# Performance work log

Hardware: AMD Instinct MI355X
Metric: run time of the kernel (lower is better)

## Reference

```python
import jax, jax.numpy as jnp
from jax import lax
import numpy as np

NUM_ANCHORS = 3
NUM_CLASSES = 20
IMG_DIM = 416.0
ANCHORS = np.array([[10.0, 13.0], [16.0, 30.0], [33.0, 23.0]], dtype=np.float32)
BN_EPS = 1e-5


def setup_inputs() -> dict:
    key = jax.random.key(0)
    ks = jax.random.split(key, 8)
    B, Cin, G = 16, 256, 52
    Cmid = 2 * Cin
    Cout = NUM_ANCHORS * (NUM_CLASSES + 5)
    # weights scaled down so exp() in the box decode stays numerically tame
    return {
        "x": jax.random.normal(ks[0], (B, Cin, G, G), jnp.float32),
        "conv1_w": jax.random.normal(ks[1], (Cmid, Cin, 3, 3), jnp.float32) * 0.05,
        "bn_gamma": jnp.ones((Cmid,), jnp.float32),
        "bn_beta": jnp.zeros((Cmid,), jnp.float32),
        "bn_mean": jax.random.normal(ks[2], (Cmid,), jnp.float32) * 0.05,
        "bn_var": jax.random.uniform(ks[3], (Cmid,), jnp.float32, 0.5, 1.5),
        "conv2_w": jax.random.normal(ks[4], (Cout, Cmid, 1, 1), jnp.float32) * 0.05,
        "conv2_b": jnp.zeros((Cout,), jnp.float32),
    }


def _conv(x, w, padding):
    return lax.conv_general_dilated(
        x, w, window_strides=(1, 1), padding=padding,
        dimension_numbers=("NCHW", "OIHW", "NCHW"))


def reference(x, conv1_w, bn_gamma, bn_beta, bn_mean, bn_var, conv2_w, conv2_b):
    # BasicConv: conv3x3 (no bias) -> BatchNorm (inference stats) -> LeakyReLU(0.1)
    y = _conv(x, conv1_w, ((1, 1), (1, 1)))
    inv = bn_gamma / jnp.sqrt(bn_var + BN_EPS)
    y = y * inv[None, :, None, None] + (bn_beta - bn_mean * inv)[None, :, None, None]
    y = jnp.where(y > 0, y, 0.1 * y)
    # 1x1 head conv with bias
    y = _conv(y, conv2_w, ((0, 0), (0, 0))) + conv2_b[None, :, None, None]

    B, G = y.shape[0], y.shape[2]
    A, NC = NUM_ANCHORS, NUM_CLASSES
    # [B, A, 5+NC, G, G] -> [B, A, G, G, 5+NC]
    pred = y.reshape(B, A, NC + 5, G, G).transpose(0, 1, 3, 4, 2)

    obj_score = jax.nn.sigmoid(pred[..., 4])        # [B,A,G,G]
    pred_cls = jax.nn.sigmoid(pred[..., 5:])        # [B,A,G,G,NC]

    stride = IMG_DIM / G
    grid = jnp.arange(G, dtype=jnp.float32)
    grid_x = grid[None, None, None, :]              # [1,1,1,G]
    grid_y = grid[None, None, :, None]              # [1,1,G,1]
    scaled = jnp.asarray(ANCHORS) / stride          # [A,2]
    anchor_w = scaled[:, 0].reshape(1, A, 1, 1)
    anchor_h = scaled[:, 1].reshape(1, A, 1, 1)

    # original uses .data (detached) for box decode
    box_in = lax.stop_gradient(pred[..., :4])
    bx = jax.nn.sigmoid(box_in[..., 0]) + grid_x
    by = jax.nn.sigmoid(box_in[..., 1]) + grid_y
    bw = jnp.exp(box_in[..., 2]) * anchor_w
    bh = jnp.exp(box_in[..., 3]) * anchor_h
    pred_boxes = jnp.stack([bx, by, bw, bh], axis=-1) * stride  # [B,A,G,G,4]

    return jnp.concatenate(
        [pred_boxes.reshape(B, -1, 4),
         obj_score.reshape(B, -1, 1),
         pred_cls.reshape(B, -1, NC)], axis=-1)
```

## Files before the change

### kernel.cpp

```cpp
#include <hip/hip_runtime.h>

typedef _Float16 f16;
typedef _Float16 f16x8 __attribute__((ext_vector_type(8)));
typedef _Float16 f16x4 __attribute__((ext_vector_type(4)));
typedef float f32x4 __attribute__((ext_vector_type(4)));

#define GDIM 52
#define GG 2704
#define CIN 256
#define CMID 512
#define COUT 75
#define NIMG 16
#define SPT 192
#define NSPB 15
#define PH 60
#define PW 54

#define AT_OFF 0
#define AT_SZ 16384
#define SLAB_OFF 65536
#define SLAB_SZ 32768

#define VMCNT(n) asm volatile("s_waitcnt vmcnt(" #n ")" ::: "memory")

__device__ __forceinline__ float sigmoidf_(float x) {
    return 1.0f / (1.0f + __expf(-x));
}

__device__ __forceinline__ void gload16(const void* g, void* l) {
    __builtin_amdgcn_global_load_lds(
        (const __attribute__((address_space(1))) unsigned int*)g,
        (__attribute__((address_space(3))) unsigned int*)l, 16, 0, 0);
}

__global__ __launch_bounds__(256) void k_zero_border(f16* __restrict__ x16p) {
    int ic = blockIdx.x;
    int tid = threadIdx.x;
    f16x8 z;
#pragma unroll
    for (int k = 0; k < 8; ++k) z[k] = (f16)0;
    for (int j = tid; j < 536; j += 256) {
        int row, col;
        if (j < 432) { int r = j / 54; row = (r == 0) ? 0 : 52 + r; col = j % 54; }
        else { int k = j - 432; row = 1 + (k >> 1); col = (k & 1) * 53; }
        f16* p = x16p + (((size_t)ic * PH + row) * PW + col) * 32;
#pragma unroll
        for (int q = 0; q < 4; ++q) *(f16x8*)(p + q * 8) = z;
    }
}

__global__ __launch_bounds__(256) void k_prep_x(const float* __restrict__ x,
                                                f16* __restrict__ x16p) {
    __shared__ float ls[32][133];
    int hw0 = blockIdx.x * 128, ck = blockIdx.y, img = blockIdx.z;
    int tid = threadIdx.x;
    const float* xb = x + ((size_t)img * CIN + ck * 32) * GG;
#pragma unroll
    for (int i = 0; i < 16; ++i) {
        int idx = tid + i * 256;
        int r = idx >> 7, c = idx & 127;
        int hw = hw0 + c;
        ls[r][c] = (hw < GG) ? xb[(size_t)r * GG + hw] : 0.0f;
    }
    __syncthreads();
    int col = tid >> 1, half = tid & 1;
    int hw = hw0 + col;
    if (hw < GG) {
        int h = hw / GDIM, w = hw % GDIM;
        f16* dst = x16p + ((((size_t)img * 8 + ck) * PH + h + 1) * PW + (w + 1)) * 32 + half * 16;
        f16x8 o0, o1;
#pragma unroll
        for (int j = 0; j < 8; ++j) o0[j] = (f16)ls[half * 16 + j][col];
#pragma unroll
        for (int j = 0; j < 8; ++j) o1[j] = (f16)ls[half * 16 + 8 + j][col];
        *(f16x8*)dst = o0;
        *(f16x8*)(dst + 8) = o1;
    }
}

__global__ __launch_bounds__(256) void k_prep_w(
    const float* __restrict__ w1, const float* __restrict__ w2,
    const float* __restrict__ gamma, const float* __restrict__ beta,
    const float* __restrict__ mean, const float* __restrict__ var,
    f16* __restrict__ w16, f16* __restrict__ w2_16,
    float* __restrict__ bnscale, float* __restrict__ bnshift) {
    int i = blockIdx.x * 256 + threadIdx.x;
    int cl = i & 31;
    int co = (i >> 5) & 511;
    int ckt = i >> 14;
    int ck = ckt & 7, tap = ckt >> 3;
    int ci = ck * 32 + cl;
    w16[i] = (f16)w1[(size_t)co * 2304 + ci * 9 + tap];
    if (i < COUT * CMID) w2_16[i] = (f16)w2[i];
    if (i < CMID) {
        float s = gamma[i] * rsqrtf(var[i] + 1e-5f);
        bnscale[i] = s;
        bnshift[i] = beta[i] - mean[i] * s;
    }
}

__global__ __launch_bounds__(512, 2) void k_conv1(
    const f16* __restrict__ x16p, const f16* __restrict__ w16,
    const float* __restrict__ bnscale, const float* __restrict__ bnshift,
    f16* __restrict__ y16) {
    __shared__ __align__(16) char smem[131072];
    int img = blockIdx.x / NSPB, sb = blockIdx.x % NSPB;
    int n0 = sb * SPT;
    int h_lo = n0 / GDIM;
    int half = blockIdx.y;
    int co0 = half * 256;
    int tid = threadIdx.x;
    int lane = tid & 63, wave = tid >> 6;
    int wm = wave >> 1, wn = wave & 1;
    int l15 = lane & 15, kg = lane >> 4;

    int roff[6];
#pragma unroll
    for (int nf = 0; nf < 6; ++nf) {
        int n = n0 + wn * 96 + nf * 16 + l15;
        int nc = n < GG ? n : GG - 1;
        int hh = nc / GDIM, ww = nc % GDIM;
        roff[nf] = ((hh - h_lo + 1) * PW + (ww + 1)) * 8;
    }

    f32x4 acc[4][6];
#pragma unroll
    for (int a = 0; a < 4; ++a)
#pragma unroll
        for (int b = 0; b < 6; ++b) {
            acc[a][b][0] = 0.f; acc[a][b][1] = 0.f;
            acc[a][b][2] = 0.f; acc[a][b][3] = 0.f;
        }

    const f16* xbase = x16p + ((size_t)img * 8 * PH + h_lo) * (PW * 32);
    f16x8 fa[2][4], fb[2][6];

    {
        const f16* wA0 = w16 + (size_t)co0 * 32;
        f16* d0 = (f16*)(smem + AT_OFF);
#pragma unroll
        for (int p = 0; p < 2; ++p) {
            int u = p * 512 + tid, s = u >> 8, c = u & 255;
            gload16(wA0 + (size_t)c * 32 + s * 8, d0 + (size_t)u * 8);
        }
        f16* sd = (f16*)(smem + SLAB_OFF);
#pragma unroll
        for (int p = 0; p < 4; ++p) {
            int cix = p * 512 + tid;
            int pix = cix & 511; if (pix > 377) pix = 377;
            gload16(xbase + (size_t)pix * 32 + (cix >> 9) * 8, sd + (size_t)cix * 8);
        }
        const f16* wA1 = w16 + ((size_t)8 * 512 + co0) * 32;
        f16* d1 = (f16*)(smem + AT_OFF + AT_SZ);
#pragma unroll
        for (int p = 0; p < 2; ++p) {
            int u = p * 512 + tid, s = u >> 8, c = u & 255;
            gload16(wA1 + (size_t)c * 32 + s * 8, d1 + (size_t)u * 8);
        }
    }
    VMCNT(2);
    __builtin_amdgcn_s_barrier();
    __builtin_amdgcn_sched_barrier(0);
    {
        const f16* Ab = (const f16*)(smem + AT_OFF);
        const f16* Sb = (const f16*)(smem + SLAB_OFF);
        const int tappix = -PW - 1;
#pragma unroll
        for (int mf = 0; mf < 4; ++mf)
            fa[0][mf] = *(const f16x8*)(Ab + kg * 2048 + (wm * 64 + l15) * 8 + mf * 128);
#pragma unroll
        for (int nf = 0; nf < 6; ++nf)
            fb[0][nf] = *(const f16x8*)(Sb + kg * 4096 + roff[nf] + tappix * 8);
    }
    __builtin_amdgcn_sched_barrier(0);

    for (int q = 0; q < 2; ++q) {
#pragma unroll
        for (int u = 0; u < 36; ++u) {
            if (u == 1 || u == 10 || u == 19 || u == 28) {
                int ckS = q * 4 + u / 9 + 1;
                const f16* sg;
                f16* sd;
                if (ckS > 7) {
                    sg = xbase + (size_t)7 * (PH * PW * 32);
                    sd = (f16*)(smem + AT_OFF + ((u + 2) % 4) * AT_SZ);
                } else {
                    sg = xbase + (size_t)ckS * (PH * PW * 32);
                    sd = (f16*)(smem + SLAB_OFF + (((u / 9) + 1) & 1) * SLAB_SZ);
                }
#pragma unroll
                for (int p = 0; p < 4; ++p) {
                    int cix = p * 512 + tid;
                    int pix = cix & 511; if (pix > 377) pix = 377;
                    gload16(sg + (size_t)pix * 32 + (cix >> 9) * 8, sd + (size_t)cix * 8);
                }
            }
            {
                const int tap2 = (u + 2) % 9;
                int ckA = q * 4 + (u + 2) / 9; if (ckA > 7) ckA = 7;
                const f16* wA = w16 + ((size_t)(tap2 * 8 + ckA) * 512 + co0) * 32;
                f16* dst = (f16*)(smem + AT_OFF + ((u + 2) % 4) * AT_SZ);
#pragma unroll
                for (int p = 0; p < 2; ++p) {
                    int uu = p * 512 + tid, s = uu >> 8, c = uu & 255;
                    gload16(wA + (size_t)c * 32 + s * 8, dst + (size_t)uu * 8);
                }
            }
            if (u == 1 || u == 10 || u == 19 || u == 28) VMCNT(6); else VMCNT(2);
            __builtin_amdgcn_s_barrier();
            __builtin_amdgcn_sched_barrier(0);
            {
                const int un = u + 1;
                const f16* Ab = (const f16*)(smem + AT_OFF + (un % 4) * AT_SZ);
                const f16* Sb = (const f16*)(smem + SLAB_OFF + ((un / 9) & 1) * SLAB_SZ);
                const int tapn = un % 9;
                const int tappix = (tapn / 3 - 1) * PW + (tapn % 3 - 1);
#pragma unroll
                for (int mf = 0; mf < 4; ++mf)
                    fa[un & 1][mf] = *(const f16x8*)(Ab + kg * 2048 +
                                                    (wm * 64 + l15) * 8 + mf * 128);
#pragma unroll
                for (int nf = 0; nf < 6; ++nf)
                    fb[un & 1][nf] = *(const f16x8*)(Sb + kg * 4096 +
                                                    roff[nf] + tappix * 8);
            }
            __builtin_amdgcn_sched_barrier(0);
            __builtin_amdgcn_s_setprio(1);
#pragma unroll
            for (int nf = 0; nf < 6; ++nf)
#pragma unroll
                for (int mf = 0; mf < 4; ++mf)
                    acc[mf][nf] = __builtin_amdgcn_mfma_f32_16x16x32_f16(
                        fa[u & 1][mf], fb[u & 1][nf], acc[mf][nf], 0, 0, 0);
            __builtin_amdgcn_s_setprio(0);
            __builtin_amdgcn_sched_barrier(0);
        }
    }
    __syncthreads();
    f16* tb = (f16*)smem;
#pragma unroll
    for (int mf = 0; mf < 4; ++mf) {
        int cr = wm * 64 + mf * 16 + kg * 4;
        f32x4 sc = *(const f32x4*)(bnscale + co0 + cr);
        f32x4 sh = *(const f32x4*)(bnshift + co0 + cr);
#pragma unroll
        for (int nf = 0; nf < 6; ++nf) {
            int pl = wn * 96 + nf * 16 + l15;
            f16x4 o;
#pragma unroll
            for (int i = 0; i < 4; ++i) {
                float v = acc[mf][nf][i] * sc[i] + sh[i];
                o[i] = (f16)(v > 0.f ? v : 0.1f * v);
            }
            *(f16x4*)(tb + pl * 264 + cr) = o;
        }
    }
    __syncthreads();
    int valid = GG - n0; if (valid > SPT) valid = SPT;
    f16* yb = y16 + (size_t)half * (NIMG * (size_t)GG * 256) + ((size_t)img * GG + n0) * 256;
#pragma unroll
    for (int p = 0; p < 12; ++p) {
        int u = p * 512 + tid, pl = u >> 5, slot = u & 31;
        if (pl < valid)
            *(f16x8*)(yb + (size_t)pl * 256 + slot * 8) =
                *(const f16x8*)(tb + pl * 264 + slot * 8);
    }
}

__global__ __launch_bounds__(256) void k_conv2(
    const f16* __restrict__ y16, const f16* __restrict__ w2_16,
    const float* __restrict__ b2, float* __restrict__ out) {
    __shared__ float ct[128][81];
    int img = blockIdx.x / 22, nb = blockIdx.x % 22;
    int n0 = nb * 128;
    int tid = threadIdx.x;
    int lane = tid & 63, wave = tid >> 6;
    int l15 = lane & 15, kg = lane >> 4;

    f32x4 acc[5][2];
#pragma unroll
    for (int a = 0; a < 5; ++a)
#pragma unroll
        for (int b = 0; b < 2; ++b) {
            acc[a][b][0] = 0.f; acc[a][b][1] = 0.f;
            acc[a][b][2] = 0.f; acc[a][b][3] = 0.f;
        }

    int nn[2];
#pragma unroll
    for (int nf = 0; nf < 2; ++nf) {
        int n = n0 + wave * 32 + nf * 16 + l15;
        nn[nf] = n < GG ? n : GG - 1;
    }
    for (int c0 = 0; c0 < CMID; c0 += 32) {
        const f16* yb = y16 + (size_t)(c0 >> 8) * (NIMG * (size_t)GG * 256) +
                        (size_t)img * GG * 256;
        int c = c0 & 255;
        f16x8 af[5];
#pragma unroll
        for (int mf = 0; mf < 5; ++mf) {
            int co = mf * 16 + l15;
            if (co < COUT)
                af[mf] = *(const f16x8*)(w2_16 + (size_t)co * CMID + c0 + kg * 8);
            else {
#pragma unroll
                for (int k = 0; k < 8; ++k) af[mf][k] = (f16)0;
            }
        }
#pragma unroll
        for (int nf = 0; nf < 2; ++nf) {
            f16x8 bf = *(const f16x8*)(yb + (size_t)nn[nf] * 256 + c + kg * 8);
#pragma unroll
            for (int mf = 0; mf < 5; ++mf)
                acc[mf][nf] = __builtin_amdgcn_mfma_f32_16x16x32_f16(
                    af[mf], bf, acc[mf][nf], 0, 0, 0);
        }
    }
#pragma unroll
    for (int mf = 0; mf < 5; ++mf)
#pragma unroll
        for (int nf = 0; nf < 2; ++nf)
            *(f32x4*)(&ct[wave * 32 + nf * 16 + l15][mf * 16 + kg * 4]) = acc[mf][nf];
    __syncthreads();
    for (int j = tid; j < 384; j += 256) {
        int a = j >> 7, nl = j & 127;
        int n = n0 + nl;
        if (n >= GG) continue;
        const float* t = &ct[nl][a * 25];
        float tv[25];
#pragma unroll
        for (int q = 0; q < 25; ++q) tv[q] = t[q] + b2[a * 25 + q];
        int h = n / GDIM, w = n % GDIM;
        const float AW[3] = {10.f, 16.f, 33.f};
        const float AH[3] = {13.f, 30.f, 23.f};
        float bx = (sigmoidf_(tv[0]) + (float)w) * 8.0f;
        float by = (sigmoidf_(tv[1]) + (float)h) * 8.0f;
        float bw_ = __expf(tv[2]) * AW[a];
        float bh_ = __expf(tv[3]) * AH[a];
        float* o = out + ((size_t)img * 8112 + (size_t)a * GG + n) * 25;
        o[0] = bx; o[1] = by; o[2] = bw_; o[3] = bh_;
        o[4] = sigmoidf_(tv[4]);
#pragma unroll
        for (int q = 0; q < 20; ++q) o[5 + q] = sigmoidf_(tv[5 + q]);
    }
}

extern "C" void kernel_launch(void* const* d_in, const int* in_sizes, int n_in,
                              void* d_out, int out_size, void* d_ws, size_t ws_size,
                              hipStream_t stream) {
    (void)in_sizes; (void)n_in; (void)out_size; (void)ws_size;
    const float* x     = (const float*)d_in[0];
    const float* w1    = (const float*)d_in[1];
    const float* gamma = (const float*)d_in[2];
    const float* beta  = (const float*)d_in[3];
    const float* mean  = (const float*)d_in[4];
    const float* var   = (const float*)d_in[5];
    const float* w2    = (const float*)d_in[6];
    const float* b2    = (const float*)d_in[7];
    float* out = (float*)d_out;

    char* ws = (char*)d_ws;
    f16* x16p     = (f16*)(ws);
    f16* w16      = (f16*)(ws + 26542080);
    f16* w2_16    = (f16*)(ws + 28901376);
    float* bnscale = (float*)(ws + 28978176);
    float* bnshift = (float*)(ws + 28980224);
    f16* y16      = (f16*)(ws + 28982272);

    k_zero_border<<<NIMG * 8, 256, 0, stream>>>(x16p);
    k_prep_x<<<dim3(22, 8, NIMG), 256, 0, stream>>>(x, x16p);
    k_prep_w<<<4608, 256, 0, stream>>>(w1, w2, gamma, beta, mean, var,
                                       w16, w2_16, bnscale, bnshift);
    k_conv1<<<dim3(NIMG * NSPB, 2), 512, 0, stream>>>(x16p, w16, bnscale,
                                                      bnshift, y16);
    k_conv2<<<NIMG * 22, 256, 0, stream>>>(y16, w2_16, b2, out);
}
```

Measured before the change: 167.6 us.

## Deepen conv1 weight prefetch to three taps ahead and restructure tap loop

Restructures the conv1 main loop into a per-input-chunk loop of templated tap bodies, and prefetches weight tiles three taps ahead instead of two, using all four LDS weight buffers. Slab loads are simplified to one clamped pixel index per thread, and wait counts are adjusted to the deeper pipeline. The aim is to hide more global-load latency behind the MFMA work, at the cost of more loads in flight and more complex buffer rotation, which could introduce hazards.

```diff
diff --git a/kernel.cpp b/kernel.cpp
--- a/kernel.cpp
+++ b/kernel.cpp
@@ -99,6 +99,62 @@
     }
 }
 
+template <int J, int CUR>
+__device__ __forceinline__ void tap_body(
+    char* smem, int ck, int co0, int tid, int spix, int a_lane, int kgx,
+    const int* __restrict__ roff, const f16* __restrict__ w16,
+    const f16* __restrict__ xbase,
+    f16x8 (&fa)[2][4], f16x8 (&fb)[2][6], f32x4 (&acc)[4][6]) {
+    if (J == 1 && ck < 7) {
+        const f16* sg = xbase + (size_t)(ck + 1) * (PH * PW * 32);
+        f16* sd = (f16*)(smem + SLAB_OFF + ((ck + 1) & 1) * SLAB_SZ);
+#pragma unroll
+        for (int p = 0; p < 4; ++p) {
+            int cix = p * 512 + tid;
+            gload16(sg + (size_t)spix * 32 + p * 8, sd + (size_t)cix * 8);
+        }
+    }
+    {
+        constexpr int tapn = (J + 3) % 9;
+        int ckn = ck + (J + 3) / 9;
+        f16* dst;
+        if (ckn > 7) { ckn = 7; dst = (f16*)(smem + SLAB_OFF); }
+        else dst = (f16*)(smem + AT_OFF + ((ck + J + 3) & 3) * AT_SZ);
+        const f16* wA = w16 + ((size_t)(tapn * 8 + ckn) * 512 + co0) * 32;
+#pragma unroll
+        for (int p = 0; p < 2; ++p) {
+            int u = p * 512 + tid;
+            gload16(wA + (size_t)(u & 255) * 32 + (u >> 8) * 8, dst + (size_t)u * 8);
+        }
+    }
+    if ((J == 1 || J == 2) && ck < 7) { VMCNT(8); } else { VMCNT(4); }
+    __builtin_amdgcn_s_barrier();
+    __builtin_amdgcn_sched_barrier(0);
+    if (!(ck == 7 && J == 8)) {
+        const f16* Ab = (const f16*)(smem + AT_OFF + ((ck + J + 1) & 3) * AT_SZ);
+        const f16* Sb = (const f16*)(smem + SLAB_OFF +
+                                     ((ck + (J == 8 ? 1 : 0)) & 1) * SLAB_SZ);
+        constexpr int TJ = (J + 1) % 9;
+        constexpr int TPXv = (TJ / 3 - 1) * PW + (TJ % 3) - 1;
+#pragma unroll
+        for (int mf = 0; mf < 4; ++mf)
+            fa[CUR ^ 1][mf] = *(const f16x8*)(Ab + a_lane + mf * 128);
+#pragma unroll
+        for (int nf = 0; nf < 6; ++nf)
+            fb[CUR ^ 1][nf] = *(const f16x8*)(Sb + kgx + roff[nf] + TPXv * 8);
+    }
+    __builtin_amdgcn_sched_barrier(0);
+    __builtin_amdgcn_s_setprio(1);
+#pragma unroll
+    for (int nf = 0; nf < 6; ++nf)
+#pragma unroll
+        for (int mf = 0; mf < 4; ++mf)
+            acc[mf][nf] = __builtin_amdgcn_mfma_f32_16x16x32_f16(
+                fa[CUR][mf], fb[CUR][nf], acc[mf][nf], 0, 0, 0);
+    __builtin_amdgcn_s_setprio(0);
+    __builtin_amdgcn_sched_barrier(0);
+}
+
 __global__ __launch_bounds__(512, 2) void k_conv1(
     const f16* __restrict__ x16p, const f16* __restrict__ w16,
     const float* __restrict__ bnscale, const float* __restrict__ bnshift,
@@ -113,6 +169,9 @@
     int lane = tid & 63, wave = tid >> 6;
     int wm = wave >> 1, wn = wave & 1;
     int l15 = lane & 15, kg = lane >> 4;
+    int a_lane = kg * 2048 + (wm * 64 + l15) * 8;
+    int kgx = kg * 4096;
+    int spix = tid < 378 ? tid : 377;
 
     int roff[6];
 #pragma unroll
@@ -140,102 +199,69 @@
         f16* d0 = (f16*)(smem + AT_OFF);
 #pragma unroll
         for (int p = 0; p < 2; ++p) {
-            int u = p * 512 + tid, s = u >> 8, c = u & 255;
-            gload16(wA0 + (size_t)c * 32 + s * 8, d0 + (size_t)u * 8);
+            int u = p * 512 + tid;
+            gload16(wA0 + (size_t)(u & 255) * 32 + (u >> 8) * 8, d0 + (size_t)u * 8);
         }
         f16* sd = (f16*)(smem + SLAB_OFF);
 #pragma unroll
         for (int p = 0; p < 4; ++p) {
             int cix = p * 512 + tid;
-            int pix = cix & 511; if (pix > 377) pix = 377;
-            gload16(xbase + (size_t)pix * 32 + (cix >> 9) * 8, sd + (size_t)cix * 8);
-        }
-        const f16* wA1 = w16 + ((size_t)8 * 512 + co0) * 32;
+            gload16(xbase + (size_t)spix * 32 + p * 8, sd + (size_t)cix * 8);
+        }
+        const f16* wA1 = w16 + ((size_t)(1 * 8) * 512 + co0) * 32;
         f16* d1 = (f16*)(smem + AT_OFF + AT_SZ);
 #pragma unroll
         for (int p = 0; p < 2; ++p) {
-            int u = p * 512 + tid, s = u >> 8, c = u & 255;
-            gload16(wA1 + (size_t)c * 32 + s * 8, d1 + (size_t)u * 8);
-        }
-    }
-    VMCNT(2);
+            int u = p * 512 + tid;
+            gload16(wA1 + (size_t)(u & 255) * 32 + (u >> 8) * 8, d1 + (size_t)u * 8);
+        }
+        const f16* wA2 = w16 + ((size_t)(2 * 8) * 512 + co0) * 32;
+        f16* d2 = (f16*)(smem + AT_OFF + 2 * AT_SZ);
+#pragma unroll
+        for (int p = 0; p < 2; ++p) {
+            int u = p * 512 + tid;
+            gload16(wA2 + (size_t)(u & 255) * 32 + (u >> 8) * 8, d2 + (size_t)u * 8);
+        }
+    }
+    VMCNT(4);
     __builtin_amdgcn_s_barrier();
     __builtin_amdgcn_sched_barrier(0);
     {
         const f16* Ab = (const f16*)(smem + AT_OFF);
         const f16* Sb = (const f16*)(smem + SLAB_OFF);
-        const int tappix = -PW - 1;
 #pragma unroll
         for (int mf = 0; mf < 4; ++mf)
-            fa[0][mf] = *(const f16x8*)(Ab + kg * 2048 + (wm * 64 + l15) * 8 + mf * 128);
+            fa[0][mf] = *(const f16x8*)(Ab + a_lane + mf * 128);
 #pragma unroll
         for (int nf = 0; nf < 6; ++nf)
-            fb[0][nf] = *(const f16x8*)(Sb + kg * 4096 + roff[nf] + tappix * 8);
+            fb[0][nf] = *(const f16x8*)(Sb + kgx + roff[nf] + (-55) * 8);
     }
     __builtin_amdgcn_sched_barrier(0);
 
-    for (int q = 0; q < 2; ++q) {
-#pragma unroll
-        for (int u = 0; u < 36; ++u) {
-            if (u == 1 || u == 10 || u == 19 || u == 28) {
-                int ckS = q * 4 + u / 9 + 1;
-                const f16* sg;
-                f16* sd;
-                if (ckS > 7) {
-                    sg = xbase + (size_t)7 * (PH * PW * 32);
-                    sd = (f16*)(smem + AT_OFF + ((u + 2) % 4) * AT_SZ);
-                } else {
-                    sg = xbase + (size_t)ckS * (PH * PW * 32);
-                    sd = (f16*)(smem + SLAB_OFF + (((u / 9) + 1) & 1) * SLAB_SZ);
-                }
-#pragma unroll
-                for (int p = 0; p < 4; ++p) {
-                    int cix = p * 512 + tid;
-                    int pix = cix & 511; if (pix > 377) pix = 377;
-                    gload16(sg + (size_t)pix * 32 + (cix >> 9) * 8, sd + (size_t)cix * 8);
-                }
-            }
-            {
-                const int tap2 = (u + 2) % 9;
-                int ckA = q * 4 + (u + 2) / 9; if (ckA > 7) ckA = 7;
-                const f16* wA = w16 + ((size_t)(tap2 * 8 + ckA) * 512 + co0) * 32;
-                f16* dst = (f16*)(smem + AT_OFF + ((u + 2) % 4) * AT_SZ);
-#pragma unroll
-                for (int p = 0; p < 2; ++p) {
-                    int uu = p * 512 + tid, s = uu >> 8, c = uu & 255;
-                    gload16(wA + (size_t)c * 32 + s * 8, dst + (size_t)uu * 8);
-                }
-            }
-            if (u == 1 || u == 10 || u == 19 || u == 28) VMCNT(6); else VMCNT(2);
-            __builtin_amdgcn_s_barrier();
-            __builtin_amdgcn_sched_barrier(0);
-            {
-                const int un = u + 1;
-                const f16* Ab = (const f16*)(smem + AT_OFF + (un % 4) * AT_SZ);
-                const f16* Sb = (const f16*)(smem + SLAB_OFF + ((un / 9) & 1) * SLAB_SZ);
-                const int tapn = un % 9;
-                const int tappix = (tapn / 3 - 1) * PW + (tapn % 3 - 1);
-#pragma unroll
-                for (int mf = 0; mf < 4; ++mf)
-                    fa[un & 1][mf] = *(const f16x8*)(Ab + kg * 2048 +
-                                                    (wm * 64 + l15) * 8 + mf * 128);
-#pragma unroll
-                for (int nf = 0; nf < 6; ++nf)
-                    fb[un & 1][nf] = *(const f16x8*)(Sb + kg * 4096 +
-                                                    roff[nf] + tappix * 8);
-            }
-            __builtin_amdgcn_sched_barrier(0);
-            __builtin_amdgcn_s_setprio(1);
-#pragma unroll
-            for (int nf = 0; nf < 6; ++nf)
-#pragma unroll
-                for (int mf = 0; mf < 4; ++mf)
-                    acc[mf][nf] = __builtin_amdgcn_mfma_f32_16x16x32_f16(
-                        fa[u & 1][mf], fb[u & 1][nf], acc[mf][nf], 0, 0, 0);
-            __builtin_amdgcn_s_setprio(0);
-            __builtin_amdgcn_sched_barrier(0);
-        }
-    }
+    for (int ck = 0; ck < 8; ++ck) {
+        if ((ck & 1) == 0) {
+            tap_body<0, 0>(smem, ck, co0, tid, spix, a_lane, kgx, roff, w16, xbase, fa, fb, acc);
+            tap_body<1, 1>(smem, ck, co0, tid, spix, a_lane, kgx, roff, w16, xbase, fa, fb, acc);
+            tap_body<2, 0>(smem, ck, co0, tid, spix, a_lane, kgx, roff, w16, xbase, fa, fb, acc);
+            tap_body<3, 1>(smem, ck, co0, tid, spix, a_lane, kgx, roff, w16, xbase, fa, fb, acc);
+            tap_body<4, 0>(smem, ck, co0, tid, spix, a_lane, kgx, roff, w16, xbase, fa, fb, acc);
+            tap_body<5, 1>(smem, ck, co0, tid, spix, a_lane, kgx, roff, w16, xbase, fa, fb, acc);
+            tap_body<6, 0>(smem, ck, co0, tid, spix, a_lane, kgx, roff, w16, xbase, fa, fb, acc);
+            tap_body<7, 1>(smem, ck, co0, tid, spix, a_lane, kgx, roff, w16, xbase, fa, fb, acc);
+            tap_body<8, 0>(smem, ck, co0, tid, spix, a_lane, kgx, roff, w16, xbase, fa, fb, acc);
+        } else {
+            tap_body<0, 1>(smem, ck, co0, tid, spix, a_lane, kgx, roff, w16, xbase, fa, fb, acc);
+            tap_body<1, 0>(smem, ck, co0, tid, spix, a_lane, kgx, roff, w16, xbase, fa, fb, acc);
+            tap_body<2, 1>(smem, ck, co0, tid, spix, a_lane, kgx, roff, w16, xbase, fa, fb, acc);
+            tap_body<3, 0>(smem, ck, co0, tid, spix, a_lane, kgx, roff, w16, xbase, fa, fb, acc);
+            tap_body<4, 1>(smem, ck, co0, tid, spix, a_lane, kgx, roff, w16, xbase, fa, fb, acc);
+            tap_body<5, 0>(smem, ck, co0, tid, spix, a_lane, kgx, roff, w16, xbase, fa, fb, acc);
+            tap_body<6, 1>(smem, ck, co0, tid, spix, a_lane, kgx, roff, w16, xbase, fa, fb, acc);
+            tap_body<7, 0>(smem, ck, co0, tid, spix, a_lane, kgx, roff, w16, xbase, fa, fb, acc);
+            tap_body<8, 1>(smem, ck, co0, tid, spix, a_lane, kgx, roff, w16, xbase, fa, fb, acc);
+        }
+    }
+    VMCNT(0);
     __syncthreads();
     f16* tb = (f16*)smem;
 #pragma unroll
```

Result: slower. 462.0 us (+175.6%).
